# Optimization experiments

Hardware: AMD Instinct MI355X
Metric: run time of the kernel (lower is better)

## Reference

```python
import jax, jax.numpy as jnp
import numpy as np

B, H, W, KS = 2, 352, 1216, 3  # KITTI depth completion, 3x3 deformable kernel


def setup_inputs() -> dict:
    key = jax.random.key(0)
    k1, k2, k3 = jax.random.split(key, 3)
    K = KS * KS
    depth = jax.random.uniform(k1, (B, 1, H, W), dtype=jnp.float32)
    weight = jax.random.uniform(k2, (B, K, H, W), dtype=jnp.float32)
    offset = jax.random.normal(k3, (B, 2 * K, H, W), dtype=jnp.float32)
    w = jnp.ones((1, 1, KS, KS), dtype=jnp.float32)  # nn.Parameter(torch.ones)
    b = jnp.zeros((1,), dtype=jnp.float32)           # nn.Parameter(torch.zeros)
    return {"depth": depth, "weight": weight, "offset": offset, "w": w, "b": b}


def _dcn_v2_post(depth, weight, offset, w, b):
    # depth: [B,1,H,W], weight(mask): [B,K,H,W], offset: [B,2K,H,W]
    Bn, _, Hn, Wn = depth.shape
    k = w.shape[-1]
    pad = (k - 1) // 2
    K = k * k
    # dkn_residual=True -> zero-mean normalize modulation over kernel channel
    weight = weight - jnp.mean(weight, axis=1, keepdims=True)
    # DCNv2 offset layout: per kernel tap idx=i*k+j, channels (2*idx, 2*idx+1) = (dy, dx)
    off = offset.reshape(Bn, K, 2, Hn, Wn)
    ky = jnp.arange(k, dtype=depth.dtype) - pad  # stride=1, dilation=1
    kyy = jnp.repeat(ky, k).reshape(1, K, 1, 1)  # row offset per tap
    kxx = jnp.tile(ky, k).reshape(1, K, 1, 1)    # col offset per tap
    py = jnp.arange(Hn, dtype=depth.dtype).reshape(1, 1, Hn, 1) + kyy + off[:, :, 0]
    px = jnp.arange(Wn, dtype=depth.dtype).reshape(1, 1, 1, Wn) + kxx + off[:, :, 1]
    y0 = jnp.floor(py)
    x0 = jnp.floor(px)
    fy = py - y0  # bilinear fractions
    fx = px - x0
    y0i = y0.astype(jnp.int32)
    x0i = x0.astype(jnp.int32)
    d_flat = depth.reshape(Bn, Hn * Wn)

    def gather(yi, xi):
        # zero-padded gather: out-of-bounds corners contribute 0 (matches DCNv2 CUDA)
        valid = (yi >= 0) & (yi < Hn) & (xi >= 0) & (xi < Wn)
        idx = jnp.clip(yi, 0, Hn - 1) * Wn + jnp.clip(xi, 0, Wn - 1)
        v = jnp.take_along_axis(d_flat, idx.reshape(Bn, -1), axis=1).reshape(idx.shape)
        return jnp.where(valid, v, jnp.zeros((), depth.dtype))

    v00 = gather(y0i, x0i)
    v01 = gather(y0i, x0i + 1)
    v10 = gather(y0i + 1, x0i)
    v11 = gather(y0i + 1, x0i + 1)
    val = (v00 * (1 - fy) * (1 - fx) + v01 * (1 - fy) * fx
           + v10 * fy * (1 - fx) + v11 * fy * fx)  # [B,K,H,W]
    # 1-in/1-out channel conv: weighted sum over K taps of (mask * sampled value)
    out = jnp.einsum('k,bkhw->bhw', w.reshape(K), weight * val)[:, None] + b[0]
    return out + depth  # dkn_residual add


def reference(depth, weight, offset, w, b):
    return _dcn_v2_post(depth, weight, offset, w, b)
```

## Files before the change

kernel.cpp:

```cpp
#include <hip/hip_runtime.h>

#define B_ 2
#define H_ 352
#define W_ 1216
#define HW_ (H_ * W_)
#define K_ 9
#define TW 64
#define TH 4
#define SOFF 8
#define SR (TH + 2 * SOFF)
#define SC (TW + 2 * SOFF)
#define NBX (W_ / TW)
#define NBY (H_ / TH)
#define NBLK (B_ * NBX * NBY)
#define NV4 (SR * (SC / 4))

typedef float v4 __attribute__((ext_vector_type(4)));

__global__ __launch_bounds__(256) void dcn_post_kernel(
    const float* __restrict__ depth,
    const float* __restrict__ weight,
    const float* __restrict__ offset,
    const float* __restrict__ wtap,
    const float* __restrict__ bias,
    float* __restrict__ out)
{
    __shared__ float sm[SR * SC];

    const int bid = blockIdx.x;
    const int b   = bid / (NBX * NBY);
    const int r2  = bid - b * (NBX * NBY);
    const int by  = r2 / NBX;
    const int bx  = r2 - by * NBX;
    const int tid = threadIdx.x;
    const int tx  = tid & (TW - 1);
    const int ty  = tid >> 6;

    const int y  = by * TH + ty;
    const int x  = bx * TW + tx;
    const int oy = by * TH - SOFF;
    const int ox = bx * TW - SOFF;
    const int p  = y * W_ + x;

    const float* __restrict__ dpt = depth + b * HW_;

#pragma unroll
    for (int i = tid; i < NV4; i += 256) {
        const int r  = i / (SC / 4);
        const int c4 = (i - r * (SC / 4)) * 4;
        const int gy = oy + r;
        const int gx = ox + c4;
        v4 v = 0.f;
        if ((unsigned)gy < (unsigned)H_ && (unsigned)gx < (unsigned)W_)
            v = *reinterpret_cast<const v4*>(dpt + gy * W_ + gx);
        *reinterpret_cast<v4*>(sm + r * SC + c4) = v;
    }

    float wt[K_];
#pragma unroll
    for (int k = 0; k < K_; ++k) wt[k] = wtap[k];
    const float bv = bias[0];

    float wg[K_];
    float m = 0.f;
    const float* wbase = weight + (size_t)b * K_ * HW_ + p;
#pragma unroll
    for (int k = 0; k < K_; ++k) {
        wg[k] = wbase[k * HW_];
        m += wg[k];
    }
    m *= (1.f / 9.f);

    float ody[K_], odx[K_];
    const float* obase = offset + (size_t)b * 2 * K_ * HW_ + p;
#pragma unroll
    for (int k = 0; k < K_; ++k) {
        ody[k] = obase[(2 * k) * HW_];
        odx[k] = obase[(2 * k + 1) * HW_];
    }

    __syncthreads();

    const float dval = sm[(ty + SOFF) * SC + (tx + SOFF)];

    float acc = 0.f;
#pragma unroll
    for (int k = 0; k < K_; ++k) {
        const float py = (float)(y + (k / 3) - 1) + ody[k];
        const float px = (float)(x + (k % 3) - 1) + odx[k];
        const float y0f = floorf(py);
        const float x0f = floorf(px);
        const float fy = py - y0f;
        const float fx = px - x0f;
        const int yi0 = (int)y0f, xi0 = (int)x0f;

        const int ly = yi0 - oy;
        const int lx = xi0 - ox;
        float v00, v01, v10, v11;
        if ((unsigned)ly <= (SR - 2) && (unsigned)lx <= (SC - 2)) {
            const float* s = sm + ly * SC + lx;
            v00 = s[0];
            v01 = s[1];
            v10 = s[SC];
            v11 = s[SC + 1];
        } else {
            const int yi1 = yi0 + 1, xi1 = xi0 + 1;
            const bool vy0 = (unsigned)yi0 < (unsigned)H_;
            const bool vy1 = (unsigned)yi1 < (unsigned)H_;
            const bool vx0 = (unsigned)xi0 < (unsigned)W_;
            const bool vx1 = (unsigned)xi1 < (unsigned)W_;
            const int r0 = yi0 * W_;
            const int r1 = r0 + W_;
            v00 = (vy0 && vx0) ? dpt[r0 + xi0] : 0.f;
            v01 = (vy0 && vx1) ? dpt[r0 + xi1] : 0.f;
            v10 = (vy1 && vx0) ? dpt[r1 + xi0] : 0.f;
            v11 = (vy1 && vx1) ? dpt[r1 + xi1] : 0.f;
        }

        const float gy = 1.f - fy, gx = 1.f - fx;
        const float val = v00 * gy * gx + v01 * gy * fx
                        + v10 * fy * gx + v11 * fy * fx;
        acc += (wg[k] - m) * wt[k] * val;
    }

    out[b * HW_ + p] = acc + bv + dval;
}

extern "C" void kernel_launch(void* const* d_in, const int* in_sizes, int n_in,
                              void* d_out, int out_size, void* d_ws, size_t ws_size,
                              hipStream_t stream) {
    const float* depth  = (const float*)d_in[0];
    const float* weight = (const float*)d_in[1];
    const float* offset = (const float*)d_in[2];
    const float* wtap   = (const float*)d_in[3];
    const float* bias   = (const float*)d_in[4];
    float* out = (float*)d_out;

    dim3 grid(NBLK), block(256);
    hipLaunchKernelGGL(dcn_post_kernel, grid, block, 0, stream,
                       depth, weight, offset, wtap, bias, out);
}
```

Baseline: 25.00 us.

## Process four tiles per block with double-buffered LDS and prefetched streams

Each block now handles four consecutive tiles. It prefetches the next tile's offset, weight and halo data into registers while computing the current tile from a second shared-memory buffer, so global load latency overlaps with compute. The bilinear blend is also rewritten as nested FMAs with precomputed per-tap coefficients. The cost is a quarter as many blocks (NTILE/TPB), more live registers, and twice the LDS per block, which may reduce occupancy and parallelism on a memory-bound kernel.

```diff
diff --git a/kernel.cpp b/kernel.cpp
--- a/kernel.cpp
+++ b/kernel.cpp
@@ -12,92 +12,112 @@
 #define SC (TW + 2 * SOFF)
 #define NBX (W_ / TW)
 #define NBY (H_ / TH)
-#define NBLK (B_ * NBX * NBY)
+#define NTILE (B_ * NBX * NBY)
+#define TPB 4
+#define NPB (NTILE / TPB)
 #define NV4 (SR * (SC / 4))
 
 typedef float v4 __attribute__((ext_vector_type(4)));
 
-__global__ __launch_bounds__(256) void dcn_post_kernel(
-    const float* __restrict__ depth,
-    const float* __restrict__ weight,
-    const float* __restrict__ offset,
-    const float* __restrict__ wtap,
-    const float* __restrict__ bias,
-    float* __restrict__ out)
-{
-    __shared__ float sm[SR * SC];
-
-    const int bid = blockIdx.x;
-    const int b   = bid / (NBX * NBY);
-    const int r2  = bid - b * (NBX * NBY);
-    const int by  = r2 / NBX;
-    const int bx  = r2 - by * NBX;
-    const int tid = threadIdx.x;
-    const int tx  = tid & (TW - 1);
-    const int ty  = tid >> 6;
-
-    const int y  = by * TH + ty;
-    const int x  = bx * TW + tx;
-    const int oy = by * TH - SOFF;
-    const int ox = bx * TW - SOFF;
-    const int p  = y * W_ + x;
-
-    const float* __restrict__ dpt = depth + b * HW_;
-
-#pragma unroll
-    for (int i = tid; i < NV4; i += 256) {
+struct Ctx { int b, oy, ox, y, x, p; };
+
+__device__ __forceinline__ Ctx mkctx(int tile, int tx, int ty) {
+    Ctx c;
+    c.b = tile / (NBX * NBY);
+    const int r  = tile - c.b * (NBX * NBY);
+    const int by = r / NBX;
+    const int bx = r - by * NBX;
+    c.oy = by * TH - SOFF;
+    c.ox = bx * TW - SOFF;
+    c.y  = by * TH + ty;
+    c.x  = bx * TW + tx;
+    c.p  = c.y * W_ + c.x;
+    return c;
+}
+
+__device__ __forceinline__ void ld_streams(const float* __restrict__ weight,
+                                           const float* __restrict__ offset,
+                                           const Ctx& c,
+                                           float* ody, float* odx, float* wg) {
+    const float* ob = offset + (size_t)c.b * 18 * HW_ + c.p;
+    const float* wb = weight + (size_t)c.b * 9 * HW_ + c.p;
+#pragma unroll
+    for (int k = 0; k < K_; ++k) {
+        ody[k] = ob[(2 * k) * HW_];
+        odx[k] = ob[(2 * k + 1) * HW_];
+    }
+#pragma unroll
+    for (int k = 0; k < K_; ++k) wg[k] = wb[k * HW_];
+}
+
+__device__ __forceinline__ void halo_load(const float* __restrict__ depth,
+                                          const Ctx& c, int tid, v4& h0, v4& h1) {
+    const float* dpt = depth + c.b * HW_;
+    {
+        const int r  = tid / (SC / 4);
+        const int c4 = (tid - r * (SC / 4)) * 4;
+        const int gy = c.oy + r, gx = c.ox + c4;
+        h0 = (v4)0.f;
+        if ((unsigned)gy < (unsigned)H_ && (unsigned)gx < (unsigned)W_)
+            h0 = *reinterpret_cast<const v4*>(dpt + gy * W_ + gx);
+    }
+    h1 = (v4)0.f;
+    if (tid < NV4 - 256) {
+        const int i  = tid + 256;
         const int r  = i / (SC / 4);
         const int c4 = (i - r * (SC / 4)) * 4;
-        const int gy = oy + r;
-        const int gx = ox + c4;
-        v4 v = 0.f;
+        const int gy = c.oy + r, gx = c.ox + c4;
         if ((unsigned)gy < (unsigned)H_ && (unsigned)gx < (unsigned)W_)
-            v = *reinterpret_cast<const v4*>(dpt + gy * W_ + gx);
-        *reinterpret_cast<v4*>(sm + r * SC + c4) = v;
-    }
-
-    float wt[K_];
-#pragma unroll
-    for (int k = 0; k < K_; ++k) wt[k] = wtap[k];
-    const float bv = bias[0];
-
-    float wg[K_];
+            h1 = *reinterpret_cast<const v4*>(dpt + gy * W_ + gx);
+    }
+}
+
+__device__ __forceinline__ void halo_write(float* sm, int tid, const v4 h0, const v4 h1) {
+    {
+        const int r  = tid / (SC / 4);
+        const int c4 = (tid - r * (SC / 4)) * 4;
+        *reinterpret_cast<v4*>(sm + r * SC + c4) = h0;
+    }
+    if (tid < NV4 - 256) {
+        const int i  = tid + 256;
+        const int r  = i / (SC / 4);
+        const int c4 = (i - r * (SC / 4)) * 4;
+        *reinterpret_cast<v4*>(sm + r * SC + c4) = h1;
+    }
+}
+
+__device__ __forceinline__ void compute_tile(const float* __restrict__ sm,
+                                             const float* __restrict__ depth,
+                                             const Ctx& c, int tx, int ty,
+                                             const float* ody, const float* odx,
+                                             const float* wg_in, const float* wt,
+                                             float bv, float* __restrict__ out) {
+    const float* dpt = depth + c.b * HW_;
+    float cf[K_];
     float m = 0.f;
-    const float* wbase = weight + (size_t)b * K_ * HW_ + p;
+#pragma unroll
+    for (int k = 0; k < K_; ++k) m += wg_in[k];
+    m *= (1.f / 9.f);
+#pragma unroll
+    for (int k = 0; k < K_; ++k) cf[k] = (wg_in[k] - m) * wt[k];
+
+    const float dval = sm[(ty + SOFF) * SC + (tx + SOFF)];
+
+    float acc = 0.f;
 #pragma unroll
     for (int k = 0; k < K_; ++k) {
-        wg[k] = wbase[k * HW_];
-        m += wg[k];
-    }
-    m *= (1.f / 9.f);
-
-    float ody[K_], odx[K_];
-    const float* obase = offset + (size_t)b * 2 * K_ * HW_ + p;
-#pragma unroll
-    for (int k = 0; k < K_; ++k) {
-        ody[k] = obase[(2 * k) * HW_];
-        odx[k] = obase[(2 * k + 1) * HW_];
-    }
-
-    __syncthreads();
-
-    const float dval = sm[(ty + SOFF) * SC + (tx + SOFF)];
-
-    float acc = 0.f;
-#pragma unroll
-    for (int k = 0; k < K_; ++k) {
-        const float py = (float)(y + (k / 3) - 1) + ody[k];
-        const float px = (float)(x + (k % 3) - 1) + odx[k];
+        const float py = (float)(c.y + (k / 3) - 1) + ody[k];
+        const float px = (float)(c.x + (k % 3) - 1) + odx[k];
         const float y0f = floorf(py);
         const float x0f = floorf(px);
         const float fy = py - y0f;
         const float fx = px - x0f;
         const int yi0 = (int)y0f, xi0 = (int)x0f;
 
-        const int ly = yi0 - oy;
-        const int lx = xi0 - ox;
+        const int ly = yi0 - c.oy;
+        const int lx = xi0 - c.ox;
         float v00, v01, v10, v11;
-        if ((unsigned)ly <= (SR - 2) && (unsigned)lx <= (SC - 2)) {
+        if (__builtin_expect((unsigned)ly <= (SR - 2) && (unsigned)lx <= (SC - 2), 1)) {
             const float* s = sm + ly * SC + lx;
             v00 = s[0];
             v01 = s[1];
@@ -117,13 +137,68 @@
             v11 = (vy1 && vx1) ? dpt[r1 + xi1] : 0.f;
         }
 
-        const float gy = 1.f - fy, gx = 1.f - fx;
-        const float val = v00 * gy * gx + v01 * gy * fx
-                        + v10 * fy * gx + v11 * fy * fx;
-        acc += (wg[k] - m) * wt[k] * val;
-    }
-
-    out[b * HW_ + p] = acc + bv + dval;
+        const float a   = fmaf(fx, v01 - v00, v00);
+        const float cc  = fmaf(fx, v11 - v10, v10);
+        const float val = fmaf(fy, cc - a, a);
+        acc = fmaf(cf[k], val, acc);
+    }
+
+    out[c.b * HW_ + c.p] = acc + bv + dval;
+}
+
+__global__ __launch_bounds__(256, 4) void dcn_post_kernel(
+    const float* __restrict__ depth,
+    const float* __restrict__ weight,
+    const float* __restrict__ offset,
+    const float* __restrict__ wtap,
+    const float* __restrict__ bias,
+    float* __restrict__ out)
+{
+    __shared__ float smA[SR * SC];
+    __shared__ float smB[SR * SC];
+
+    const int tid = threadIdx.x;
+    const int tx  = tid & (TW - 1);
+    const int ty  = tid >> 6;
+    const int t0  = blockIdx.x * TPB;
+
+    float wt[K_];
+#pragma unroll
+    for (int k = 0; k < K_; ++k) wt[k] = wtap[k];
+    const float bv = bias[0];
+
+    float odyA[K_], odxA[K_], wgA[K_];
+    float odyB[K_], odxB[K_], wgB[K_];
+    v4 h0, h1;
+
+    Ctx cA = mkctx(t0 + 0, tx, ty);
+    ld_streams(weight, offset, cA, odyA, odxA, wgA);
+    halo_load(depth, cA, tid, h0, h1);
+    halo_write(smA, tid, h0, h1);
+    __syncthreads();
+
+    Ctx cB = mkctx(t0 + 1, tx, ty);
+    ld_streams(weight, offset, cB, odyB, odxB, wgB);
+    halo_load(depth, cB, tid, h0, h1);
+    compute_tile(smA, depth, cA, tx, ty, odyA, odxA, wgA, wt, bv, out);
+    halo_write(smB, tid, h0, h1);
+    __syncthreads();
+
+    cA = mkctx(t0 + 2, tx, ty);
+    ld_streams(weight, offset, cA, odyA, odxA, wgA);
+    halo_load(depth, cA, tid, h0, h1);
+    compute_tile(smB, depth, cB, tx, ty, odyB, odxB, wgB, wt, bv, out);
+    halo_write(smA, tid, h0, h1);
+    __syncthreads();
+
+    cB = mkctx(t0 + 3, tx, ty);
+    ld_streams(weight, offset, cB, odyB, odxB, wgB);
+    halo_load(depth, cB, tid, h0, h1);
+    compute_tile(smA, depth, cA, tx, ty, odyA, odxA, wgA, wt, bv, out);
+    halo_write(smB, tid, h0, h1);
+    __syncthreads();
+
+    compute_tile(smB, depth, cB, tx, ty, odyB, odxB, wgB, wt, bv, out);
 }
 
 extern "C" void kernel_launch(void* const* d_in, const int* in_sizes, int n_in,
@@ -136,7 +211,7 @@
     const float* bias   = (const float*)d_in[4];
     float* out = (float*)d_out;
 
-    dim3 grid(NBLK), block(256);
+    dim3 grid(NPB), block(256);
     hipLaunchKernelGGL(dcn_post_kernel, grid, block, 0, stream,
                        depth, weight, offset, wtap, bias, out);
 }
```

Measured after the change: 28.91 us. 15.7% more time.
